# Kernel tuning notes

Hardware: AMD Instinct MI355X
Metric: run time of the kernel (lower is better)

## Reference

```python
import jax, jax.numpy as jnp
import numpy as np

N_NODES = 50000
N_GRAPHS = 64


def _gcn_layer(x, w, b, src, dst, dinv):
    # GCNConv: out = D^{-1/2} (A+I) D^{-1/2} (x W) + b; self-loops already in src/dst
    xw = x @ w                                  # [N, out]
    norm = (dinv[src] * dinv[dst])[:, None]     # [E+N, 1]
    msgs = xw[src] * norm                       # gather + scale
    out = jax.ops.segment_sum(msgs, dst, num_segments=N_NODES)
    return out + b


def setup_inputs() -> dict:
    key = jax.random.key(0)
    ks = jax.random.split(key, 12)
    E = 800000
    F_IN, H = 128, 256
    x = jax.random.normal(ks[0], (N_NODES, F_IN), dtype=jnp.float32)
    edge_attr = jax.random.normal(ks[1], (E, 4), dtype=jnp.float32)
    edge_index = jax.random.randint(ks[2], (2, E), 0, N_NODES, dtype=jnp.int64)
    batch = jnp.sort(jax.random.randint(ks[3], (N_NODES,), 0, N_GRAPHS, dtype=jnp.int64))
    def glorot(k, fi, fo):
        s = jnp.sqrt(6.0 / (fi + fo))
        return jax.random.uniform(k, (fi, fo), minval=-s, maxval=s, dtype=jnp.float32)
    return {
        "x": x, "edge_attr": edge_attr, "edge_index": edge_index, "batch": batch,
        "w1": glorot(ks[4], F_IN, H), "b1": jnp.zeros((H,), jnp.float32),
        "w2": glorot(ks[5], H, H), "b2": jnp.zeros((H,), jnp.float32),
        "w3": glorot(ks[6], H, H), "b3": jnp.zeros((H,), jnp.float32),
        "lin1_w": glorot(ks[7], H, H // 2), "lin1_b": jnp.zeros((H // 2,), jnp.float32),
        "lin2_w": glorot(ks[8], H // 2, 3), "lin2_b": jnp.zeros((3,), jnp.float32),
    }


def reference(x, edge_attr, edge_index, batch, w1, b1, w2, b2, w3, b3,
              lin1_w, lin1_b, lin2_w, lin2_b):
    # add self-loops once; shared by all three conv layers
    loop = jnp.arange(N_NODES, dtype=edge_index.dtype)
    src = jnp.concatenate([edge_index[0], loop])
    dst = jnp.concatenate([edge_index[1], loop])
    deg = jax.ops.segment_sum(jnp.ones_like(dst, dtype=x.dtype), dst, num_segments=N_NODES)
    dinv = jnp.where(deg > 0, jax.lax.rsqrt(deg), 0.0)

    h = jax.nn.relu(_gcn_layer(x, w1, b1, src, dst, dinv))
    h = jax.nn.relu(_gcn_layer(h, w2, b2, src, dst, dinv))
    h = _gcn_layer(h, w3, b3, src, dst, dinv)

    # global mean pool over graphs
    sums = jax.ops.segment_sum(h, batch, num_segments=N_GRAPHS)
    cnts = jax.ops.segment_sum(jnp.ones((h.shape[0],), h.dtype), batch, num_segments=N_GRAPHS)
    pooled = sums / jnp.maximum(cnts, 1.0)[:, None]

    # eval mode: dropout is identity
    out = pooled @ lin1_w + lin1_b
    out = out @ lin2_w + lin2_b
    return out
```

## Files before the change

### kernel.cpp

```cpp
#include <hip/hip_runtime.h>
#include <cstdint>

constexpr int NG = 64;
constexpr int H  = 256;

typedef __bf16 bf16x8 __attribute__((ext_vector_type(8)));
typedef float  f32x4  __attribute__((ext_vector_type(4)));

__device__ __forceinline__ uint32_t pk_bf16(float a, float b) {
    uint32_t ua = __builtin_bit_cast(uint32_t, a);
    uint32_t ub = __builtin_bit_cast(uint32_t, b);
    ua += 0x7fffu + ((ua >> 16) & 1u);
    ub += 0x7fffu + ((ub >> 16) & 1u);
    return (ua >> 16) | (ub & 0xffff0000u);
}
__device__ __forceinline__ ushort bf16r(float x) {
    uint32_t u = __builtin_bit_cast(uint32_t, x);
    u += 0x7fffu + ((u >> 16) & 1u);
    return (ushort)(u >> 16);
}
__device__ __forceinline__ float bf2f(ushort h) {
    return __builtin_bit_cast(float, ((uint32_t)h) << 16);
}
__device__ __forceinline__ void bf2acc(uint32_t u, float& a0, float& a1) {
    a0 += __builtin_bit_cast(float, u << 16);
    a1 += __builtin_bit_cast(float, u & 0xffff0000u);
}

__global__ void hist_kernel(const int* __restrict__ dst, int* __restrict__ cnt, int E) {
    int e = blockIdx.x * blockDim.x + threadIdx.x;
    if (e < E) atomicAdd(&cnt[dst[e]], 1);
}

__global__ __launch_bounds__(256) void scanA(const int* __restrict__ cnt, int* __restrict__ bsum,
                                             float* __restrict__ dinv, int n) {
    __shared__ int sh[256];
    int t = threadIdx.x, i = blockIdx.x * 256 + t;
    int v = (i < n) ? cnt[i] : 0;
    if (i < n) dinv[i] = rsqrtf((float)(v + 1));
    sh[t] = v;
    __syncthreads();
    for (int off = 128; off > 0; off >>= 1) {
        if (t < off) sh[t] += sh[t + off];
        __syncthreads();
    }
    if (t == 0) bsum[blockIdx.x] = sh[0];
}

__global__ __launch_bounds__(256) void scanB(const int* __restrict__ bsum, int* __restrict__ boff,
                                             int* __restrict__ total_out, int nb,
                                             float* __restrict__ sums, int* __restrict__ gcnt) {
    __shared__ int sh[256];
    int t = threadIdx.x;
    for (int i = t; i < NG * H; i += 256) sums[i] = 0.f;
    if (t < NG) gcnt[t] = 0;
    int v = (t < nb) ? bsum[t] : 0;
    sh[t] = v;
    __syncthreads();
    for (int off = 1; off < 256; off <<= 1) {
        int a = (t >= off) ? sh[t - off] : 0;
        __syncthreads();
        sh[t] += a;
        __syncthreads();
    }
    if (t < nb) boff[t] = sh[t] - v;
    if (t == nb - 1) *total_out = sh[t];
}

__global__ __launch_bounds__(256) void scanC(const int* __restrict__ cnt, const int* __restrict__ boff,
                                             int* __restrict__ row_ptr, int* __restrict__ fill, int n) {
    __shared__ int sh[256];
    int t = threadIdx.x, i = blockIdx.x * 256 + t;
    int v = (i < n) ? cnt[i] : 0;
    sh[t] = v;
    __syncthreads();
    for (int off = 1; off < 256; off <<= 1) {
        int a = (t >= off) ? sh[t - off] : 0;
        __syncthreads();
        sh[t] += a;
        __syncthreads();
    }
    if (i < n) {
        int excl = boff[blockIdx.x] + sh[t] - v;
        row_ptr[i] = excl;
        fill[i] = excl;
    }
}

constexpr int WCONV_BLOCKS = (128 * 256 + 256 * 256) / 256;
__global__ void wsp_kernel(const float* __restrict__ w1, ushort* __restrict__ h1, ushort* __restrict__ l1,
                           const float* __restrict__ w2, ushort* __restrict__ h2, ushort* __restrict__ l2,
                           const int* __restrict__ src, const int* __restrict__ dst,
                           int* __restrict__ fill, ushort* __restrict__ ssrc, int E,
                           const float* __restrict__ x, const float* __restrict__ dinv,
                           ushort* __restrict__ y, int N) {
    if (blockIdx.x < WCONV_BLOCKS) {
        int idx = blockIdx.x * 256 + threadIdx.x;
        const float* w; ushort *hi, *lo; int K;
        if (idx < 128 * 256) { w = w1; hi = h1; lo = l1; K = 128; }
        else { idx -= 128 * 256; w = w2; hi = h2; lo = l2; K = 256; }
        int k = idx / 256, n = idx & 255;
        float v = w[idx];
        ushort h = bf16r(v);
        float r = v - bf2f(h);
        hi[n * K + k] = h;
        lo[n * K + k] = bf16r(r);
        return;
    }
    int i = (blockIdx.x - WCONV_BLOCKS) * 256 + threadIdx.x;
    if (i < E) {
        int pos = atomicAdd(&fill[dst[i]], 1);
        ssrc[pos] = (ushort)src[i];
    }
    int np4 = N * 32;
    if (i < np4) {
        int f = i * 4;
        int node = f >> 7;
        int k = f & 127;
        float dv = dinv[node];
        float4 v = *reinterpret_cast<const float4*>(x + f);
        uint2 o;
        o.x = pk_bf16(v.x * dv, v.y * dv);
        o.y = pk_bf16(v.z * dv, v.w * dv);
        *reinterpret_cast<uint2*>(y + ((size_t)(k >> 5) * N + node) * 32 + (k & 31)) = o;
    }
}

template<int NC>
__global__ __launch_bounds__(256) void agg_kernel(const ushort* __restrict__ y,
                                                  const float* __restrict__ dinv,
                                                  const int* __restrict__ row_ptr,
                                                  const ushort* __restrict__ ssrc,
                                                  ushort* __restrict__ zout, int n) {
    int wave = threadIdx.x >> 6;
    int lane = threadIdx.x & 63;
    int grp  = lane >> 3;
    int fd   = lane & 7;
    int chunk = blockIdx.x % NC;
    int node  = (blockIdx.x / NC) * 32 + wave * 8 + grp;
    if (node >= n) return;
    const ushort* yc = y + (size_t)chunk * n * 32;

    float a0, a1, a2, a3;
    {
        uint2 u = *reinterpret_cast<const uint2*>(yc + (size_t)node * 32 + fd * 4);
        a0 = a1 = a2 = a3 = 0.f;
        bf2acc(u.x, a0, a1); bf2acc(u.y, a2, a3);
    }
    int beg = row_ptr[node], end = row_ptr[node + 1];
    int e = beg;
    for (; e + 2 <= end; e += 2) {
        int s0 = ssrc[e], s1 = ssrc[e + 1];
        uint2 u0 = *reinterpret_cast<const uint2*>(yc + (size_t)s0 * 32 + fd * 4);
        uint2 u1 = *reinterpret_cast<const uint2*>(yc + (size_t)s1 * 32 + fd * 4);
        bf2acc(u0.x, a0, a1); bf2acc(u0.y, a2, a3);
        bf2acc(u1.x, a0, a1); bf2acc(u1.y, a2, a3);
    }
    if (e < end) {
        int s = ssrc[e];
        uint2 u = *reinterpret_cast<const uint2*>(yc + (size_t)s * 32 + fd * 4);
        bf2acc(u.x, a0, a1); bf2acc(u.y, a2, a3);
    }
    float dv = dinv[node];
    uint2 o;
    o.x = pk_bf16(dv * a0, dv * a1);
    o.y = pk_bf16(dv * a2, dv * a3);
    *reinterpret_cast<uint2*>(zout + ((size_t)chunk * n + node) * 32 + fd * 4) = o;
}

template<bool RELU>
__global__ __launch_bounds__(256) void mfma_gemm(const ushort* __restrict__ A,
                                                 const ushort* __restrict__ Bhi,
                                                 const ushort* __restrict__ Blo,
                                                 const float* __restrict__ bias,
                                                 const float* __restrict__ dinv,
                                                 ushort* __restrict__ C, int M, int K) {
    constexpr int BM = 128, BN = 64, BK = 64;
    constexpr int LDK = BK + 8;
    __shared__ ushort As[BM][LDK];
    __shared__ ushort Bh[BN][LDK];
    __shared__ ushort Bl[BN][LDK];

    const int tid = threadIdx.x;
    const int w = tid >> 6;
    const int l = tid & 63;
    const int lr = l & 15;
    const int lk = (l >> 4) * 8;
    const int bm = blockIdx.x * BM;
    const int bn = blockIdx.y * BN;

    f32x4 acc[8];
    #pragma unroll
    for (int i = 0; i < 8; ++i) acc[i] = (f32x4){0.f, 0.f, 0.f, 0.f};

    for (int k0 = 0; k0 < K; k0 += BK) {
        #pragma unroll
        for (int p = 0; p < 4; ++p) {
            int g = tid + p * 256;
            int r = g >> 3;
            int c = (g & 7) << 3;
            int grow = bm + r;
            int gk = k0 + c;
            uint4 va = make_uint4(0u, 0u, 0u, 0u);
            if (grow < M)
                va = *reinterpret_cast<const uint4*>(A + ((size_t)(gk >> 5) * M + grow) * 32 + (gk & 31));
            *reinterpret_cast<uint4*>(&As[r][c]) = va;
        }
        #pragma unroll
        for (int p = 0; p < 2; ++p) {
            int g = tid + p * 256;
            int r = g >> 3;
            int c = (g & 7) << 3;
            *reinterpret_cast<uint4*>(&Bh[r][c]) =
                *reinterpret_cast<const uint4*>(Bhi + (size_t)(bn + r) * K + k0 + c);
            *reinterpret_cast<uint4*>(&Bl[r][c]) =
                *reinterpret_cast<const uint4*>(Blo + (size_t)(bn + r) * K + k0 + c);
        }
        __syncthreads();
        #pragma unroll
        for (int kk = 0; kk < BK; kk += 32) {
            bf16x8 bh = *reinterpret_cast<const bf16x8*>(&Bh[w * 16 + lr][kk + lk]);
            bf16x8 bl = *reinterpret_cast<const bf16x8*>(&Bl[w * 16 + lr][kk + lk]);
            #pragma unroll
            for (int r16 = 0; r16 < 8; ++r16) {
                bf16x8 a = *reinterpret_cast<const bf16x8*>(&As[r16 * 16 + lr][kk + lk]);
                acc[r16] = __builtin_amdgcn_mfma_f32_16x16x32_bf16(a, bh, acc[r16], 0, 0, 0);
                acc[r16] = __builtin_amdgcn_mfma_f32_16x16x32_bf16(a, bl, acc[r16], 0, 0, 0);
            }
        }
        __syncthreads();
    }

    int col = bn + w * 16 + lr;
    int cc = col >> 5, co = col & 31;
    float bv = bias[col];
    #pragma unroll
    for (int r16 = 0; r16 < 8; ++r16) {
        #pragma unroll
        for (int j = 0; j < 4; ++j) {
            int row = bm + r16 * 16 + (l >> 4) * 4 + j;
            if (row < M) {
                float v = acc[r16][j] + bv;
                if (RELU) v = fmaxf(v, 0.f);
                v *= dinv[row];
                C[((size_t)cc * M + row) * 32 + co] = bf16r(v);
            }
        }
    }
}

__global__ __launch_bounds__(256) void pool_kernel(const ushort* __restrict__ z,
                                                   const int* __restrict__ batch,
                                                   float* __restrict__ sums,
                                                   int* __restrict__ gcnt, int n) {
    constexpr int NCH = 128;
    int t = threadIdx.x;
    int base = blockIdx.x * NCH;
    if (base >= n) return;
    int endn = min(base + NCH, n);
    size_t poff = (size_t)(t >> 5) * n;
    int co = t & 31;
    int cur = batch[base];
    float local = 0.f;
    int cl = 0;
    for (int i = base; i < endn; ++i) {
        int g = batch[i];
        if (g != cur) {
            atomicAdd(&sums[cur * H + t], local);
            if (t == 0) atomicAdd(&gcnt[cur], cl);
            local = 0.f; cl = 0; cur = g;
        }
        local += bf2f(z[(poff + i) * 32 + co]);
        cl++;
    }
    atomicAdd(&sums[cur * H + t], local);
    if (t == 0) atomicAdd(&gcnt[cur], cl);
}

__global__ __launch_bounds__(256) void head_kernel(const float* __restrict__ sums,
                                                   const int* __restrict__ gcnt,
                                                   const float* __restrict__ w3, const float* __restrict__ b3,
                                                   const float* __restrict__ l1w, const float* __restrict__ l1b,
                                                   const float* __restrict__ l2w, const float* __restrict__ l2b,
                                                   float* __restrict__ out) {
    __shared__ float pooled[H];
    __shared__ float t3[H];
    __shared__ float mid[H / 2];
    int g = blockIdx.x, t = threadIdx.x;
    float c = (float)max(gcnt[g], 1);
    pooled[t] = sums[g * H + t] / c;
    __syncthreads();
    float a = b3[t];
    for (int k = 0; k < H; ++k) a += pooled[k] * w3[k * H + t];
    t3[t] = a;
    __syncthreads();
    if (t < H / 2) {
        float m = l1b[t];
        for (int k = 0; k < H; ++k) m += t3[k] * l1w[k * (H / 2) + t];
        mid[t] = m;
    }
    __syncthreads();
    if (t < 3) {
        float o = l2b[t];
        for (int k = 0; k < H / 2; ++k) o += mid[k] * l2w[k * 3 + t];
        out[g * 3 + t] = o;
    }
}

extern "C" void kernel_launch(void* const* d_in, const int* in_sizes, int n_in,
                              void* d_out, int out_size, void* d_ws, size_t ws_size,
                              hipStream_t stream) {
    const float* x   = (const float*)d_in[0];
    const int*   ei  = (const int*)d_in[2];
    const int*   bat = (const int*)d_in[3];
    const float* w1  = (const float*)d_in[4];
    const float* b1  = (const float*)d_in[5];
    const float* w2  = (const float*)d_in[6];
    const float* b2  = (const float*)d_in[7];
    const float* w3  = (const float*)d_in[8];
    const float* b3  = (const float*)d_in[9];
    const float* l1w = (const float*)d_in[10];
    const float* l1b = (const float*)d_in[11];
    const float* l2w = (const float*)d_in[12];
    const float* l2b = (const float*)d_in[13];
    float* out = (float*)d_out;

    const int N = in_sizes[0] / 128;
    const int E = in_sizes[2] / 2;
    const int NB = (N + 255) / 256;

    char* ws = (char*)d_ws;
    size_t off = 0;
    auto alloc = [&](size_t bytes) {
        void* p = ws + off;
        off = (off + bytes + 255) & ~(size_t)255;
        return p;
    };
    ushort* yb     = (ushort*)alloc((size_t)N * H * 2);
    ushort* z16    = (ushort*)alloc((size_t)N * H * 2);
    int*    cnt    = (int*)alloc((size_t)N * 4);
    float*  dinv   = (float*)alloc((size_t)N * 4);
    int*    row_ptr= (int*)alloc((size_t)(N + 1) * 4);
    int*    fill   = (int*)alloc((size_t)N * 4);
    ushort* ssrc   = (ushort*)alloc((size_t)E * 2);
    int*    bsum   = (int*)alloc(256 * 4);
    int*    boff   = (int*)alloc(256 * 4);
    ushort* wt1h   = (ushort*)alloc((size_t)128 * 256 * 2);
    ushort* wt1l   = (ushort*)alloc((size_t)128 * 256 * 2);
    ushort* wt2h   = (ushort*)alloc((size_t)256 * 256 * 2);
    ushort* wt2l   = (ushort*)alloc((size_t)256 * 256 * 2);
    float*  sums   = (float*)alloc((size_t)NG * H * 4);
    int*    gcnt   = (int*)alloc((size_t)NG * 4);

    hipMemsetAsync(cnt, 0, (size_t)N * 4, stream);

    hist_kernel<<<(E + 255) / 256, 256, 0, stream>>>(ei + E, cnt, E);
    scanA<<<NB, 256, 0, stream>>>(cnt, bsum, dinv, N);
    scanB<<<1, 256, 0, stream>>>(bsum, boff, row_ptr + N, NB, sums, gcnt);
    scanC<<<NB, 256, 0, stream>>>(cnt, boff, row_ptr, fill, N);
    int sp_blocks = (N * 32 + 255) / 256;
    wsp_kernel<<<WCONV_BLOCKS + sp_blocks, 256, 0, stream>>>(
        w1, wt1h, wt1l, w2, wt2h, wt2l,
        ei, ei + E, fill, ssrc, E, x, dinv, yb, N);

    const int AGG_BLOCKS = (N + 31) / 32;
    agg_kernel<4><<<AGG_BLOCKS * 4, 256, 0, stream>>>(yb, dinv, row_ptr, ssrc, z16, N);
    mfma_gemm<true><<<dim3((N + 127) / 128, 4), 256, 0, stream>>>(z16, wt1h, wt1l, b1, dinv, yb, N, 128);

    agg_kernel<8><<<AGG_BLOCKS * 8, 256, 0, stream>>>(yb, dinv, row_ptr, ssrc, z16, N);
    mfma_gemm<true><<<dim3((N + 127) / 128, 4), 256, 0, stream>>>(z16, wt2h, wt2l, b2, dinv, yb, N, 256);

    agg_kernel<8><<<AGG_BLOCKS * 8, 256, 0, stream>>>(yb, dinv, row_ptr, ssrc, z16, N);

    pool_kernel<<<(N + 127) / 128, 256, 0, stream>>>(z16, bat, sums, gcnt, N);
    head_kernel<<<NG, 256, 0, stream>>>(sums, gcnt, w3, b3, l1w, l1b, l2w, l2b, out);
}
```

Measured before the change: 470.5 us.

## Fold final GCN aggregation into pooling via per-node graph coefficient matrix

Because mean pooling is linear, the third layer's sparse aggregation is replaced by a precomputed coefficient matrix c[node][graph]. Each entry sums dinv[dst] over edges from that node into the graph (plus the self-loop), and the matrix is built with atomics during CSR construction. A new pooling kernel weights each node's pre-aggregation features by these coefficients, removing one full agg pass and the old pool kernel. Graph counts now come from binary search on the sorted batch array, and the agg inner loop is unrolled by 4. The cost is an N×64 float matrix that must be zeroed and filled, plus 850k float atomics.

```diff
diff --git a/kernel.cpp b/kernel.cpp
--- a/kernel.cpp
+++ b/kernel.cpp
@@ -26,6 +26,11 @@
     a0 += __builtin_bit_cast(float, u << 16);
     a1 += __builtin_bit_cast(float, u & 0xffff0000u);
 }
+__device__ __forceinline__ int lower_bound(const int* a, int n, int v) {
+    int lo = 0, hi = n;
+    while (lo < hi) { int m = (lo + hi) >> 1; if (a[m] < v) lo = m + 1; else hi = m; }
+    return lo;
+}
 
 __global__ void hist_kernel(const int* __restrict__ dst, int* __restrict__ cnt, int E) {
     int e = blockIdx.x * blockDim.x + threadIdx.x;
@@ -33,11 +38,17 @@
 }
 
 __global__ __launch_bounds__(256) void scanA(const int* __restrict__ cnt, int* __restrict__ bsum,
-                                             float* __restrict__ dinv, int n) {
+                                             float* __restrict__ dinv, float* __restrict__ c, int n) {
     __shared__ int sh[256];
     int t = threadIdx.x, i = blockIdx.x * 256 + t;
     int v = (i < n) ? cnt[i] : 0;
-    if (i < n) dinv[i] = rsqrtf((float)(v + 1));
+    if (i < n) {
+        dinv[i] = rsqrtf((float)(v + 1));
+        float4 z4 = make_float4(0.f, 0.f, 0.f, 0.f);
+        float4* cp = reinterpret_cast<float4*>(c + (size_t)i * NG);
+        #pragma unroll
+        for (int q = 0; q < NG / 4; ++q) cp[q] = z4;
+    }
     sh[t] = v;
     __syncthreads();
     for (int off = 128; off > 0; off >>= 1) {
@@ -49,11 +60,10 @@
 
 __global__ __launch_bounds__(256) void scanB(const int* __restrict__ bsum, int* __restrict__ boff,
                                              int* __restrict__ total_out, int nb,
-                                             float* __restrict__ sums, int* __restrict__ gcnt) {
+                                             float* __restrict__ sums) {
     __shared__ int sh[256];
     int t = threadIdx.x;
     for (int i = t; i < NG * H; i += 256) sums[i] = 0.f;
-    if (t < NG) gcnt[t] = 0;
     int v = (t < nb) ? bsum[t] : 0;
     sh[t] = v;
     __syncthreads();
@@ -93,6 +103,7 @@
                            const int* __restrict__ src, const int* __restrict__ dst,
                            int* __restrict__ fill, ushort* __restrict__ ssrc, int E,
                            const float* __restrict__ x, const float* __restrict__ dinv,
+                           const int* __restrict__ bat, float* __restrict__ c,
                            ushort* __restrict__ y, int N) {
     if (blockIdx.x < WCONV_BLOCKS) {
         int idx = blockIdx.x * 256 + threadIdx.x;
@@ -102,15 +113,19 @@
         int k = idx / 256, n = idx & 255;
         float v = w[idx];
         ushort h = bf16r(v);
-        float r = v - bf2f(h);
         hi[n * K + k] = h;
-        lo[n * K + k] = bf16r(r);
+        lo[n * K + k] = bf16r(v - bf2f(h));
         return;
     }
     int i = (blockIdx.x - WCONV_BLOCKS) * 256 + threadIdx.x;
     if (i < E) {
-        int pos = atomicAdd(&fill[dst[i]], 1);
-        ssrc[pos] = (ushort)src[i];
+        int s = src[i], d = dst[i];
+        int pos = atomicAdd(&fill[d], 1);
+        ssrc[pos] = (ushort)s;
+        atomicAdd(&c[(size_t)s * NG + bat[d]], dinv[d]);
+    }
+    if (i < N) {
+        atomicAdd(&c[(size_t)i * NG + bat[i]], dinv[i]);
     }
     int np4 = N * 32;
     if (i < np4) {
@@ -149,14 +164,18 @@
     }
     int beg = row_ptr[node], end = row_ptr[node + 1];
     int e = beg;
-    for (; e + 2 <= end; e += 2) {
-        int s0 = ssrc[e], s1 = ssrc[e + 1];
+    for (; e + 4 <= end; e += 4) {
+        int s0 = ssrc[e], s1 = ssrc[e + 1], s2 = ssrc[e + 2], s3 = ssrc[e + 3];
         uint2 u0 = *reinterpret_cast<const uint2*>(yc + (size_t)s0 * 32 + fd * 4);
         uint2 u1 = *reinterpret_cast<const uint2*>(yc + (size_t)s1 * 32 + fd * 4);
+        uint2 u2 = *reinterpret_cast<const uint2*>(yc + (size_t)s2 * 32 + fd * 4);
+        uint2 u3 = *reinterpret_cast<const uint2*>(yc + (size_t)s3 * 32 + fd * 4);
         bf2acc(u0.x, a0, a1); bf2acc(u0.y, a2, a3);
         bf2acc(u1.x, a0, a1); bf2acc(u1.y, a2, a3);
-    }
-    if (e < end) {
+        bf2acc(u2.x, a0, a1); bf2acc(u2.y, a2, a3);
+        bf2acc(u3.x, a0, a1); bf2acc(u3.y, a2, a3);
+    }
+    for (; e < end; ++e) {
         int s = ssrc[e];
         uint2 u = *reinterpret_cast<const uint2*>(yc + (size_t)s * 32 + fd * 4);
         bf2acc(u.x, a0, a1); bf2acc(u.y, a2, a3);
@@ -249,36 +268,36 @@
     }
 }
 
-__global__ __launch_bounds__(256) void pool_kernel(const ushort* __restrict__ z,
-                                                   const int* __restrict__ batch,
-                                                   float* __restrict__ sums,
-                                                   int* __restrict__ gcnt, int n) {
-    constexpr int NCH = 128;
+__global__ __launch_bounds__(256) void pg_kernel(const ushort* __restrict__ y,
+                                                 const float* __restrict__ c,
+                                                 float* __restrict__ sums, int n) {
+    constexpr int TN = 512;
+    int chunk = blockIdx.x & 7;
+    int base  = (blockIdx.x >> 3) * TN;
+    if (base >= n) return;
+    int endn = min(base + TN, n);
     int t = threadIdx.x;
-    int base = blockIdx.x * NCH;
-    if (base >= n) return;
-    int endn = min(base + NCH, n);
-    size_t poff = (size_t)(t >> 5) * n;
-    int co = t & 31;
-    int cur = batch[base];
-    float local = 0.f;
-    int cl = 0;
+    int g = t >> 2;
+    int q = t & 3;
+    const ushort* yp = y + (size_t)chunk * n * 32;
+    float acc[8] = {};
     for (int i = base; i < endn; ++i) {
-        int g = batch[i];
-        if (g != cur) {
-            atomicAdd(&sums[cur * H + t], local);
-            if (t == 0) atomicAdd(&gcnt[cur], cl);
-            local = 0.f; cl = 0; cur = g;
-        }
-        local += bf2f(z[(poff + i) * 32 + co]);
-        cl++;
-    }
-    atomicAdd(&sums[cur * H + t], local);
-    if (t == 0) atomicAdd(&gcnt[cur], cl);
+        float cv = c[(size_t)i * NG + g];
+        uint4 u = *reinterpret_cast<const uint4*>(yp + (size_t)i * 32 + q * 8);
+        float f0, f1, f2, f3, f4, f5, f6, f7;
+        f0 = f1 = f2 = f3 = f4 = f5 = f6 = f7 = 0.f;
+        bf2acc(u.x, f0, f1); bf2acc(u.y, f2, f3);
+        bf2acc(u.z, f4, f5); bf2acc(u.w, f6, f7);
+        acc[0] += cv * f0; acc[1] += cv * f1; acc[2] += cv * f2; acc[3] += cv * f3;
+        acc[4] += cv * f4; acc[5] += cv * f5; acc[6] += cv * f6; acc[7] += cv * f7;
+    }
+    float* sp = sums + g * H + chunk * 32 + q * 8;
+    #pragma unroll
+    for (int k = 0; k < 8; ++k) atomicAdd(&sp[k], acc[k]);
 }
 
 __global__ __launch_bounds__(256) void head_kernel(const float* __restrict__ sums,
-                                                   const int* __restrict__ gcnt,
+                                                   const int* __restrict__ bat, int n,
                                                    const float* __restrict__ w3, const float* __restrict__ b3,
                                                    const float* __restrict__ l1w, const float* __restrict__ l1b,
                                                    const float* __restrict__ l2w, const float* __restrict__ l2b,
@@ -287,8 +306,10 @@
     __shared__ float t3[H];
     __shared__ float mid[H / 2];
     int g = blockIdx.x, t = threadIdx.x;
-    float c = (float)max(gcnt[g], 1);
-    pooled[t] = sums[g * H + t] / c;
+    int lo = lower_bound(bat, n, g);
+    int hi = lower_bound(bat, n, g + 1);
+    float cdeg = (float)max(hi - lo, 1);
+    pooled[t] = sums[g * H + t] / cdeg;
     __syncthreads();
     float a = b3[t];
     for (int k = 0; k < H; ++k) a += pooled[k] * w3[k * H + t];
@@ -338,6 +359,7 @@
     };
     ushort* yb     = (ushort*)alloc((size_t)N * H * 2);
     ushort* z16    = (ushort*)alloc((size_t)N * H * 2);
+    float*  cmat   = (float*)alloc((size_t)N * NG * 4);
     int*    cnt    = (int*)alloc((size_t)N * 4);
     float*  dinv   = (float*)alloc((size_t)N * 4);
     int*    row_ptr= (int*)alloc((size_t)(N + 1) * 4);
@@ -350,18 +372,17 @@
     ushort* wt2h   = (ushort*)alloc((size_t)256 * 256 * 2);
     ushort* wt2l   = (ushort*)alloc((size_t)256 * 256 * 2);
     float*  sums   = (float*)alloc((size_t)NG * H * 4);
-    int*    gcnt   = (int*)alloc((size_t)NG * 4);
 
     hipMemsetAsync(cnt, 0, (size_t)N * 4, stream);
 
     hist_kernel<<<(E + 255) / 256, 256, 0, stream>>>(ei + E, cnt, E);
-    scanA<<<NB, 256, 0, stream>>>(cnt, bsum, dinv, N);
-    scanB<<<1, 256, 0, stream>>>(bsum, boff, row_ptr + N, NB, sums, gcnt);
+    scanA<<<NB, 256, 0, stream>>>(cnt, bsum, dinv, cmat, N);
+    scanB<<<1, 256, 0, stream>>>(bsum, boff, row_ptr + N, NB, sums);
     scanC<<<NB, 256, 0, stream>>>(cnt, boff, row_ptr, fill, N);
     int sp_blocks = (N * 32 + 255) / 256;
     wsp_kernel<<<WCONV_BLOCKS + sp_blocks, 256, 0, stream>>>(
         w1, wt1h, wt1l, w2, wt2h, wt2l,
-        ei, ei + E, fill, ssrc, E, x, dinv, yb, N);
+        ei, ei + E, fill, ssrc, E, x, dinv, bat, cmat, yb, N);
 
     const int AGG_BLOCKS = (N + 31) / 32;
     agg_kernel<4><<<AGG_BLOCKS * 4, 256, 0, stream>>>(yb, dinv, row_ptr, ssrc, z16, N);
@@ -370,8 +391,6 @@
     agg_kernel<8><<<AGG_BLOCKS * 8, 256, 0, stream>>>(yb, dinv, row_ptr, ssrc, z16, N);
     mfma_gemm<true><<<dim3((N + 127) / 128, 4), 256, 0, stream>>>(z16, wt2h, wt2l, b2, dinv, yb, N, 256);
 
-    agg_kernel<8><<<AGG_BLOCKS * 8, 256, 0, stream>>>(yb, dinv, row_ptr, ssrc, z16, N);
-
-    pool_kernel<<<(N + 127) / 128, 256, 0, stream>>>(z16, bat, sums, gcnt, N);
-    head_kernel<<<NG, 256, 0, stream>>>(sums, gcnt, w3, b3, l1w, l1b, l2w, l2b, out);
-}
+    pg_kernel<<<((N + 511) / 512) * 8, 256, 0, stream>>>(yb, cmat, sums, N);
+    head_kernel<<<NG, 256, 0, stream>>>(sums, bat, N, w3, b3, l1w, l1b, l2w, l2b, out);
+}
```

After: 615.1 us. 1.31x slower.
